# Performance work log

Measured on AMD Instinct MI355X. Metric: run time of the kernel, lower is better.

## Reference

```python
import jax, jax.numpy as jnp
import numpy as np

S = 7
B = 2
C = 20
LAMBDA_NOOBJ = 0.5
EPS = 1e-9  # guards IoU division; original divides by raw union


def setup_inputs() -> dict:
    key = jax.random.key(0)
    k1, k2 = jax.random.split(key)
    N = 8192
    preds = jax.random.uniform(k1, (N, S, S, B * (5 + C)), dtype=jnp.float32)
    targets = jax.random.uniform(k2, (N, S, S, B * (5 + C)), dtype=jnp.float32)
    return {"preds": preds, "targets": targets}


def _iou_xywh(a, b):
    # a, b: (..., 4) in (cx, cy, w, h); returns (...,) IoU
    ax1 = a[..., 0] - a[..., 2] / 2
    ay1 = a[..., 1] - a[..., 3] / 2
    ax2 = a[..., 0] + a[..., 2] / 2
    ay2 = a[..., 1] + a[..., 3] / 2
    bx1 = b[..., 0] - b[..., 2] / 2
    by1 = b[..., 1] - b[..., 3] / 2
    bx2 = b[..., 0] + b[..., 2] / 2
    by2 = b[..., 1] + b[..., 3] / 2
    iw = jnp.clip(jnp.minimum(ax2, bx2) - jnp.maximum(ax1, bx1), 0.0)
    ih = jnp.clip(jnp.minimum(ay2, by2) - jnp.maximum(ay1, by1), 0.0)
    inter = iw * ih
    union = a[..., 2] * a[..., 3] + b[..., 2] * b[..., 3] - inter
    return inter / (union + EPS)


def reference(preds, targets):
    N = preds.shape[0]
    p = preds.reshape(N, S, S, B, 5 + C)
    t = targets.reshape(N, S, S, B, 5 + C)

    # per-cell, per-slot IoU between pred box b and target box b: (N,S,S,B)
    ious = _iou_xywh(p[..., :4], t[..., :4])

    # best-box selection per cell
    best = jnp.argmax(ious, axis=-1)                       # (N,S,S)
    best_oh = jax.nn.one_hot(best, B, dtype=preds.dtype)   # (N,S,S,B)

    # object presence from target confidence of any box slot
    has_object = jnp.any(t[..., 4] > 0.0, axis=-1)         # (N,S,S)

    # 1) position loss (x,y) for the responsible box in object cells
    dxy = jnp.sum((p[..., 0:2] - t[..., 0:2]) ** 2, axis=-1)     # (N,S,S,B)
    pos_loss = jnp.sum(best_oh * dxy, axis=-1)                   # (N,S,S)
    loss = jnp.sum(jnp.where(has_object, pos_loss, 0.0))

    # 2) class loss (last C entries of the cell vector) for every cell
    pc = p[..., -1, 5:]   # (N,S,S,C)
    tc = t[..., -1, 5:]
    loss = loss + jnp.sum((pc - tc) ** 2)

    # 3) confidence loss: pred_conf = iou_b * p_class[gt], target_conf = iou_b
    gt_cls = jnp.argmax(tc, axis=-1)                                    # (N,S,S)
    p_gt = jnp.take_along_axis(pc, gt_cls[..., None], axis=-1)[..., 0]  # (N,S,S)
    conf_err = (ious * p_gt[..., None] - ious) ** 2                     # (N,S,S,B)
    w = jnp.where(best_oh > 0, 1.0, LAMBDA_NOOBJ)
    loss = loss + jnp.sum(w * conf_err)

    return loss / N
```

## Files before the change

kernel.cpp:

```cpp
#include <hip/hip_runtime.h>


#define NPC 50
#define CPT 64
#define TPB 64
#define TILE_F (CPT * NPC)
#define NCHUNK 28

typedef const __attribute__((address_space(1))) void gvoid_t;
typedef __attribute__((address_space(3))) void lvoid_t;

__device__ __forceinline__ float iou_xywh(float px, float py, float pw, float ph,
                                          float tx, float ty, float tw, float th) {
    float ax1 = px - pw * 0.5f, ay1 = py - ph * 0.5f;
    float ax2 = px + pw * 0.5f, ay2 = py + ph * 0.5f;
    float bx1 = tx - tw * 0.5f, by1 = ty - th * 0.5f;
    float bx2 = tx + tw * 0.5f, by2 = ty + th * 0.5f;
    float iw = fmaxf(fminf(ax2, bx2) - fmaxf(ax1, bx1), 0.0f);
    float ih = fmaxf(fminf(ay2, by2) - fmaxf(ay1, by1), 0.0f);
    float inter = iw * ih;
    float uni = pw * ph + tw * th - inter;
    return inter / (uni + 1e-9f);
}

__device__ __forceinline__ float cell_loss(const float2* __restrict__ cp2,
                                           const float2* __restrict__ ct2) {
    float2 p01 = cp2[0];
    float2 p23 = cp2[1];
    float2 t01 = ct2[0];
    float2 t23 = ct2[1];
    float2 t4_ = ct2[2];
    float2 pA = cp2[12];
    float2 pB = cp2[13];
    float2 pC = cp2[14];
    float2 tA = ct2[12];
    float2 tB = ct2[13];
    float2 tC = ct2[14];

    float iou0 = iou_xywh(p01.x, p01.y, p23.x, p23.y,
                          t01.x, t01.y, t23.x, t23.y);
    float iou1 = iou_xywh(pA.y, pB.x, pB.y, pC.x,
                          tA.y, tB.x, tB.y, tC.x);
    int best = (iou1 > iou0) ? 1 : 0;
    bool has_obj = (t4_.x > 0.0f) || (tC.y > 0.0f);

    float dx, dy;
    if (best == 0) { dx = p01.x - t01.x; dy = p01.y - t01.y; }
    else           { dx = pA.y - tA.y;   dy = pB.x - tB.x;   }
    float cell = has_obj ? (dx * dx + dy * dy) : 0.0f;

    float csum = 0.0f;
    float bv = -1e30f;
    float pg = 0.0f;
    #pragma unroll
    for (int j = 0; j < 10; ++j) {
        float2 tv = ct2[15 + j];
        float2 pv = cp2[15 + j];
        float d0 = pv.x - tv.x;
        float d1 = pv.y - tv.y;
        csum += d0 * d0 + d1 * d1;
        if (tv.x > bv) { bv = tv.x; pg = pv.x; }
        if (tv.y > bv) { bv = tv.y; pg = pv.y; }
    }
    cell += csum;

    float f = pg - 1.0f;
    float f2 = f * f;
    float e0 = iou0 * iou0 * f2;
    float e1 = iou1 * iou1 * f2;
    cell += (best == 0) ? e0 : 0.5f * e0;
    cell += (best == 1) ? e1 : 0.5f * e1;
    return cell;
}

__global__ __launch_bounds__(TPB) void yolo_cell_kernel(
        const float* __restrict__ preds,
        const float* __restrict__ targets,
        float* __restrict__ part,
        int ncells, int nb) {
    __shared__ float lbuf[2][2 * TILE_F];

    const int lane = threadIdx.x;
    const int bid = blockIdx.x;
    const int ntiles = ncells / CPT;

    float acc = 0.0f;

    auto stage = [&](int b, int t) {
        const float* ps = preds + (long long)t * TILE_F;
        const float* ts = targets + (long long)t * TILE_F;
        float* lp = lbuf[b];
        float* lt = lbuf[b] + TILE_F;
        #pragma unroll
        for (int c = 0; c < 12; ++c)
            __builtin_amdgcn_global_load_lds((gvoid_t*)(ps + c * 256 + lane * 4),
                                             (lvoid_t*)(lp + c * 256), 16, 0, 0);
        #pragma unroll
        for (int c = 0; c < 2; ++c)
            __builtin_amdgcn_global_load_lds((gvoid_t*)(ps + 3072 + c * 64 + lane),
                                             (lvoid_t*)(lp + 3072 + c * 64), 4, 0, 0);
        #pragma unroll
        for (int c = 0; c < 12; ++c)
            __builtin_amdgcn_global_load_lds((gvoid_t*)(ts + c * 256 + lane * 4),
                                             (lvoid_t*)(lt + c * 256), 16, 0, 0);
        #pragma unroll
        for (int c = 0; c < 2; ++c)
            __builtin_amdgcn_global_load_lds((gvoid_t*)(ts + 3072 + c * 64 + lane),
                                             (lvoid_t*)(lt + 3072 + c * 64), 4, 0, 0);
    };

    if (bid < ntiles) stage(0, bid);
    int b = 0;
    for (int t = bid; t < ntiles; t += nb) {
        const int tn = t + nb;
        if (tn < ntiles) {
            stage(b ^ 1, tn);
            asm volatile("s_waitcnt vmcnt(28)" ::: "memory");
        } else {
            asm volatile("s_waitcnt vmcnt(0)" ::: "memory");
        }
        __builtin_amdgcn_sched_barrier(0);

        const float2* cp2 = (const float2*)(lbuf[b] + lane * NPC);
        const float2* ct2 = (const float2*)(lbuf[b] + TILE_F + lane * NPC);
        acc += cell_loss(cp2, ct2);
        b ^= 1;
    }

    const int rem0 = ntiles * CPT;
    if (rem0 < ncells && bid == nb - 1) {
        for (int i = rem0 + lane; i < ncells; i += TPB) {
            const float2* cp2 = (const float2*)(preds + (long long)i * NPC);
            const float2* ct2 = (const float2*)(targets + (long long)i * NPC);
            acc += cell_loss(cp2, ct2);
        }
    }

    #pragma unroll
    for (int off = 32; off >= 1; off >>= 1) acc += __shfl_down(acc, off);
    if (lane == 0) part[bid] = acc;
}

__global__ __launch_bounds__(256) void yolo_final_kernel(
        const float* __restrict__ part, float* __restrict__ out,
        int nblk, float invN) {
    __shared__ float wsum[4];
    const int tid = threadIdx.x;
    float s = 0.0f;
    for (int i = tid; i < nblk; i += 256) s += part[i];
    #pragma unroll
    for (int off = 32; off >= 1; off >>= 1) s += __shfl_down(s, off);
    if ((tid & 63) == 0) wsum[tid >> 6] = s;
    __syncthreads();
    if (tid == 0) {
        out[0] = (wsum[0] + wsum[1] + wsum[2] + wsum[3]) * invN;
    }
}

extern "C" void kernel_launch(void* const* d_in, const int* in_sizes, int n_in,
                              void* d_out, int out_size, void* d_ws, size_t ws_size,
                              hipStream_t stream) {
    const float* preds = (const float*)d_in[0];
    const float* targets = (const float*)d_in[1];
    float* out = (float*)d_out;
    float* part = (float*)d_ws;

    const int ncells = in_sizes[0] / NPC;
    const int N = ncells / 49;
    const int nb = 768;

    yolo_cell_kernel<<<nb, TPB, 0, stream>>>(preds, targets, part, ncells, nb);
    yolo_final_kernel<<<1, 256, 0, stream>>>(part, out, nb, 1.0f / (float)N);
}
```

Baseline: 31.10 us.

## Split each cell across two lanes and halve tile size with doubled grid

New measurement: 32.82 us. 1.06x slower.

```diff
diff --git a/kernel.cpp b/kernel.cpp
--- a/kernel.cpp
+++ b/kernel.cpp
@@ -2,10 +2,9 @@
 
 
 #define NPC 50
-#define CPT 64
+#define CPT 32
 #define TPB 64
 #define TILE_F (CPT * NPC)
-#define NCHUNK 28
 
 typedef const __attribute__((address_space(1))) void gvoid_t;
 typedef __attribute__((address_space(3))) void lvoid_t;
@@ -25,22 +24,13 @@
 
 __device__ __forceinline__ float cell_loss(const float2* __restrict__ cp2,
                                            const float2* __restrict__ ct2) {
-    float2 p01 = cp2[0];
-    float2 p23 = cp2[1];
-    float2 t01 = ct2[0];
-    float2 t23 = ct2[1];
-    float2 t4_ = ct2[2];
-    float2 pA = cp2[12];
-    float2 pB = cp2[13];
-    float2 pC = cp2[14];
-    float2 tA = ct2[12];
-    float2 tB = ct2[13];
-    float2 tC = ct2[14];
+    float2 p01 = cp2[0], p23 = cp2[1];
+    float2 t01 = ct2[0], t23 = ct2[1], t4_ = ct2[2];
+    float2 pA = cp2[12], pB = cp2[13], pC = cp2[14];
+    float2 tA = ct2[12], tB = ct2[13], tC = ct2[14];
 
-    float iou0 = iou_xywh(p01.x, p01.y, p23.x, p23.y,
-                          t01.x, t01.y, t23.x, t23.y);
-    float iou1 = iou_xywh(pA.y, pB.x, pB.y, pC.x,
-                          tA.y, tB.x, tB.y, tC.x);
+    float iou0 = iou_xywh(p01.x, p01.y, p23.x, p23.y, t01.x, t01.y, t23.x, t23.y);
+    float iou1 = iou_xywh(pA.y, pB.x, pB.y, pC.x, tA.y, tB.x, tB.y, tC.x);
     int best = (iou1 > iou0) ? 1 : 0;
     bool has_obj = (t4_.x > 0.0f) || (tC.y > 0.0f);
 
@@ -49,25 +39,20 @@
     else           { dx = pA.y - tA.y;   dy = pB.x - tB.x;   }
     float cell = has_obj ? (dx * dx + dy * dy) : 0.0f;
 
-    float csum = 0.0f;
-    float bv = -1e30f;
-    float pg = 0.0f;
+    float csum = 0.0f, bv = -1e30f, pg = 0.0f;
     #pragma unroll
     for (int j = 0; j < 10; ++j) {
         float2 tv = ct2[15 + j];
         float2 pv = cp2[15 + j];
-        float d0 = pv.x - tv.x;
-        float d1 = pv.y - tv.y;
+        float d0 = pv.x - tv.x, d1 = pv.y - tv.y;
         csum += d0 * d0 + d1 * d1;
         if (tv.x > bv) { bv = tv.x; pg = pv.x; }
         if (tv.y > bv) { bv = tv.y; pg = pv.y; }
     }
     cell += csum;
 
-    float f = pg - 1.0f;
-    float f2 = f * f;
-    float e0 = iou0 * iou0 * f2;
-    float e1 = iou1 * iou1 * f2;
+    float f = pg - 1.0f, f2 = f * f;
+    float e0 = iou0 * iou0 * f2, e1 = iou1 * iou1 * f2;
     cell += (best == 0) ? e0 : 0.5f * e0;
     cell += (best == 1) ? e1 : 0.5f * e1;
     return cell;
@@ -81,6 +66,8 @@
     __shared__ float lbuf[2][2 * TILE_F];
 
     const int lane = threadIdx.x;
+    const int odd = lane & 1;
+    const int c = lane >> 1;
     const int bid = blockIdx.x;
     const int ntiles = ncells / CPT;
 
@@ -92,21 +79,17 @@
         float* lp = lbuf[b];
         float* lt = lbuf[b] + TILE_F;
         #pragma unroll
-        for (int c = 0; c < 12; ++c)
-            __builtin_amdgcn_global_load_lds((gvoid_t*)(ps + c * 256 + lane * 4),
-                                             (lvoid_t*)(lp + c * 256), 16, 0, 0);
+        for (int k = 0; k < 6; ++k)
+            __builtin_amdgcn_global_load_lds((gvoid_t*)(ps + k * 256 + lane * 4),
+                                             (lvoid_t*)(lp + k * 256), 16, 0, 0);
+        __builtin_amdgcn_global_load_lds((gvoid_t*)(ps + 1536 + lane),
+                                         (lvoid_t*)(lp + 1536), 4, 0, 0);
         #pragma unroll
-        for (int c = 0; c < 2; ++c)
-            __builtin_amdgcn_global_load_lds((gvoid_t*)(ps + 3072 + c * 64 + lane),
-                                             (lvoid_t*)(lp + 3072 + c * 64), 4, 0, 0);
-        #pragma unroll
-        for (int c = 0; c < 12; ++c)
-            __builtin_amdgcn_global_load_lds((gvoid_t*)(ts + c * 256 + lane * 4),
-                                             (lvoid_t*)(lt + c * 256), 16, 0, 0);
-        #pragma unroll
-        for (int c = 0; c < 2; ++c)
-            __builtin_amdgcn_global_load_lds((gvoid_t*)(ts + 3072 + c * 64 + lane),
-                                             (lvoid_t*)(lt + 3072 + c * 64), 4, 0, 0);
+        for (int k = 0; k < 6; ++k)
+            __builtin_amdgcn_global_load_lds((gvoid_t*)(ts + k * 256 + lane * 4),
+                                             (lvoid_t*)(lt + k * 256), 16, 0, 0);
+        __builtin_amdgcn_global_load_lds((gvoid_t*)(ts + 1536 + lane),
+                                         (lvoid_t*)(lt + 1536), 4, 0, 0);
     };
 
     if (bid < ntiles) stage(0, bid);
@@ -115,15 +98,56 @@
         const int tn = t + nb;
         if (tn < ntiles) {
             stage(b ^ 1, tn);
-            asm volatile("s_waitcnt vmcnt(28)" ::: "memory");
+            asm volatile("s_waitcnt vmcnt(14)" ::: "memory");
         } else {
             asm volatile("s_waitcnt vmcnt(0)" ::: "memory");
         }
         __builtin_amdgcn_sched_barrier(0);
 
-        const float2* cp2 = (const float2*)(lbuf[b] + lane * NPC);
-        const float2* ct2 = (const float2*)(lbuf[b] + TILE_F + lane * NPC);
-        acc += cell_loss(cp2, ct2);
+        const float2* cp2 = (const float2*)(lbuf[b] + c * NPC);
+        const float2* ct2 = (const float2*)(lbuf[b] + TILE_F + c * NPC);
+
+        float iou0 = 0.0f, iou1 = 0.0f, dxy = 0.0f;
+        int best = 0;
+        bool has_obj = false;
+        float csum = 0.0f, pg = 0.0f;
+        if (!odd) {
+            float2 p01 = cp2[0], p23 = cp2[1];
+            float2 t01 = ct2[0], t23 = ct2[1], t4_ = ct2[2];
+            float2 pA = cp2[12], pB = cp2[13], pC = cp2[14];
+            float2 tA = ct2[12], tB = ct2[13], tC = ct2[14];
+            iou0 = iou_xywh(p01.x, p01.y, p23.x, p23.y,
+                            t01.x, t01.y, t23.x, t23.y);
+            iou1 = iou_xywh(pA.y, pB.x, pB.y, pC.x,
+                            tA.y, tB.x, tB.y, tC.x);
+            best = (iou1 > iou0) ? 1 : 0;
+            has_obj = (t4_.x > 0.0f) || (tC.y > 0.0f);
+            float dx, dy;
+            if (best == 0) { dx = p01.x - t01.x; dy = p01.y - t01.y; }
+            else           { dx = pA.y - tA.y;   dy = pB.x - tB.x;   }
+            dxy = dx * dx + dy * dy;
+        } else {
+            float bv = -1e30f;
+            #pragma unroll
+            for (int j = 0; j < 10; ++j) {
+                float2 tv = ct2[15 + j];
+                float2 pv = cp2[15 + j];
+                float d0 = pv.x - tv.x, d1 = pv.y - tv.y;
+                csum += d0 * d0 + d1 * d1;
+                if (tv.x > bv) { bv = tv.x; pg = pv.x; }
+                if (tv.y > bv) { bv = tv.y; pg = pv.y; }
+            }
+        }
+        float pgx = __shfl_xor(pg, 1);
+        float csx = __shfl_xor(csum, 1);
+        if (!odd) {
+            float cell = (has_obj ? dxy : 0.0f) + csx;
+            float f = pgx - 1.0f, f2 = f * f;
+            float e0 = iou0 * iou0 * f2, e1 = iou1 * iou1 * f2;
+            cell += (best == 0) ? e0 : 0.5f * e0;
+            cell += (best == 1) ? e1 : 0.5f * e1;
+            acc += cell;
+        }
         b ^= 1;
     }
 
@@ -167,7 +191,7 @@
 
     const int ncells = in_sizes[0] / NPC;
     const int N = ncells / 49;
-    const int nb = 768;
+    const int nb = 1536;
 
     yolo_cell_kernel<<<nb, TPB, 0, stream>>>(preds, targets, part, ncells, nb);
     yolo_final_kernel<<<1, 256, 0, stream>>>(part, out, nb, 1.0f / (float)N);
```
